# Kernel tuning notes

Hardware: AMD Instinct MI355X
Metric: run time of the kernel (lower is better)

The kernel has to match this reference:

```python
import jax, jax.numpy as jnp
import numpy as np

VOCAB, EMB, WIN = 32000, 300, 5
H1, H2, NY, NZ = 300, 300, 128, 128
B, S = 32, 512


def setup_inputs() -> dict:
    key = jax.random.key(0)
    ks = jax.random.split(key, 16)
    sc = 0.05
    inp = {
        "x": jax.random.randint(ks[0], (B, S, WIN), 0, VOCAB),
        "emb": jax.random.normal(ks[1], (VOCAB, EMB), jnp.float32) * sc,
        "W_ih1": jax.random.normal(ks[2], (H1, EMB * WIN), jnp.float32) * sc,
        "W_hh1": jax.random.normal(ks[3], (H1, H1), jnp.float32) * sc,
        "b_ih1": jax.random.normal(ks[4], (H1,), jnp.float32) * sc,
        "b_hh1": jax.random.normal(ks[5], (H1,), jnp.float32) * sc,
        "W_ih2": jax.random.normal(ks[6], (H2, H1), jnp.float32) * sc,
        "W_hh2": jax.random.normal(ks[7], (H2, H2), jnp.float32) * sc,
        "b_ih2": jax.random.normal(ks[8], (H2,), jnp.float32) * sc,
        "b_hh2": jax.random.normal(ks[9], (H2,), jnp.float32) * sc,
        "fc1_w": jax.random.normal(ks[10], (NY, H1), jnp.float32) * sc,
        "fc1_b": jax.random.normal(ks[11], (NY,), jnp.float32) * sc,
        "fc2_w": jax.random.normal(ks[12], (NZ, H2), jnp.float32) * sc,
        "fc2_b": jax.random.normal(ks[13], (NZ,), jnp.float32) * sc,
    }
    return inp


def reference(x, emb, W_ih1, W_hh1, b_ih1, b_hh1, W_ih2, W_hh2, b_ih2, b_hh2,
              fc1_w, fc1_b, fc2_w, fc2_b):
    b, s, w = x.shape
    xe = emb[jnp.transpose(x, (1, 0, 2))].reshape(s, b, w * emb.shape[1])
    xe = jax.nn.relu(xe)

    h1_0 = jnp.zeros((b, W_hh1.shape[0]), xe.dtype)
    h2_0 = jnp.zeros((b, W_hh2.shape[0]), xe.dtype)

    def step(carry, xt):
        h1, h2 = carry
        h1 = jnp.tanh(xt @ W_ih1.T + b_ih1 + h1 @ W_hh1.T + b_hh1)
        h2 = jnp.tanh(h1 @ W_ih2.T + b_ih2 + h2 @ W_hh2.T + b_hh2)
        return (h1, h2), (h1, h2)

    _, (out1, out2) = jax.lax.scan(step, (h1_0, h2_0), xe)  # [S,B,H]

    out1 = jnp.transpose(out1, (1, 0, 2)).reshape(b * s, -1)
    out2 = jnp.transpose(out2, (1, 0, 2)).reshape(b * s, -1)
    out1 = out1 @ fc1_w.T + fc1_b
    out2 = out2 @ fc2_w.T + fc2_b
    return (out1, out2)
```

## Files before the change

### kernel.cpp

```cpp
#include <hip/hip_runtime.h>
#include <hip/hip_fp16.h>

#define S_LEN 512
#define BATCH 32
#define CHUNK 16

typedef _Float16 hv2  __attribute__((ext_vector_type(2)));
typedef _Float16 half8 __attribute__((ext_vector_type(8)));
typedef float    f32x4 __attribute__((ext_vector_type(4)));

__device__ __forceinline__ float dot2f(hv2 a, hv2 b, float c) {
#if __has_builtin(__builtin_amdgcn_fdot2)
    return __builtin_amdgcn_fdot2(a, b, c, false);
#else
    return c + (float)a.x * (float)b.x + (float)a.y * (float)b.y;
#endif
}

__device__ __forceinline__ float fast_tanh(float x) {
    float e = __expf(2.f * x);
    return 1.f - 2.f / (e + 1.f);
}

__device__ __forceinline__ void lds_barrier() {
    __asm__ volatile("s_waitcnt lgkmcnt(0)\n\ts_barrier" ::: "memory");
}
__device__ __forceinline__ void vm_drain() {
    __asm__ volatile("s_waitcnt vmcnt(0)" ::: "memory");
}

#define F_GC0 64

#define E8   1280000
#define W18  64000
#define W28  12800
#define FF8  5120
#define PREP_TOTAL8 (E8 + W18 + W28 + FF8 + FF8)

__global__ __launch_bounds__(256) void k_prep(
    const float* __restrict__ emb,  const float* __restrict__ Wih1,
    const float* __restrict__ Wih2, const float* __restrict__ fc1w,
    const float* __restrict__ fc2w,
    _Float16* __restrict__ embf, _Float16* __restrict__ Wf1,
    _Float16* __restrict__ Wf2,  _Float16* __restrict__ F1,
    _Float16* __restrict__ F2,   unsigned int* __restrict__ flags)
{
    int gid = blockIdx.x * 256 + threadIdx.x;
    if (gid < 128) flags[gid] = 0u;
    if (gid >= PREP_TOTAL8) return;

    half8 v;
    _Float16* dst;

    if (gid < E8) {
        int row = gid / 40, c8 = (gid - row * 40) * 8;
        #pragma unroll
        for (int j = 0; j < 8; ++j) {
            int c = c8 + j;
            float f = (c < 300) ? emb[(size_t)row * 300 + c] : 0.f;
            v[j] = (_Float16)(f > 0.f ? f : 0.f);
        }
        dst = embf + (size_t)gid * 8;
    } else if (gid < E8 + W18) {
        int i = gid - E8;
        int row = i / 200, c8 = (i - row * 200) * 8;
        #pragma unroll
        for (int j = 0; j < 8; ++j) {
            int c = c8 + j, w = c / 320, cc = c - w * 320;
            float f = (row < 300 && cc < 300) ? Wih1[(size_t)row * 1500 + w * 300 + cc] : 0.f;
            v[j] = (_Float16)f;
        }
        dst = Wf1 + (size_t)i * 8;
    } else if (gid < E8 + W18 + W28) {
        int i = gid - E8 - W18;
        int row = i / 40, c8 = (i - row * 40) * 8;
        #pragma unroll
        for (int j = 0; j < 8; ++j) {
            int c = c8 + j;
            float f = (row < 300 && c < 300) ? Wih2[(size_t)row * 300 + c] : 0.f;
            v[j] = (_Float16)f;
        }
        dst = Wf2 + (size_t)i * 8;
    } else if (gid < E8 + W18 + W28 + FF8) {
        int i = gid - E8 - W18 - W28;
        int row = i / 40, c8 = (i - row * 40) * 8;
        #pragma unroll
        for (int j = 0; j < 8; ++j) {
            int c = c8 + j;
            v[j] = (_Float16)((c < 300) ? fc1w[(size_t)row * 300 + c] : 0.f);
        }
        dst = F1 + (size_t)i * 8;
    } else {
        int i = gid - E8 - W18 - W28 - FF8;
        int row = i / 40, c8 = (i - row * 40) * 8;
        #pragma unroll
        for (int j = 0; j < 8; ++j) {
            int c = c8 + j;
            v[j] = (_Float16)((c < 300) ? fc2w[(size_t)row * 300 + c] : 0.f);
        }
        dst = F2 + (size_t)i * 8;
    }
    *(half8*)dst = v;
}

#define LDS_BYTES 52096
#define NREC 64
#define NGEMM 76

__device__ __forceinline__ void load_u_regs(float* up, const float* __restrict__ U1,
                                            int b, int t0) {
    #pragma unroll
    for (int j = 0; j < 10; ++j) {
        int e = threadIdx.x + 512 * j;
        int row = e / 300, col = e - row * 300;
        up[j] = (e < 4800) ? U1[((size_t)((t0 + row) * BATCH + b)) * 300 + col] : 0.f;
    }
}

__device__ __forceinline__ void wait_gemm(unsigned int* flags, int c) {
    if (threadIdx.x == 0) {
        while (__hip_atomic_load(&flags[F_GC0 + c], __ATOMIC_ACQUIRE,
                                 __HIP_MEMORY_SCOPE_AGENT) < (unsigned)NGEMM)
            __builtin_amdgcn_s_sleep(2);
    }
    __syncthreads();
}

__device__ __forceinline__ void fc_epilogue(
    const _Float16 (*hc)[320], const _Float16* __restrict__ F,
    const float* __restrict__ fb, float* __restrict__ out,
    int b, int tb, int wid, int lm, int lq)
{
    f32x4 acc = (f32x4){0.f, 0.f, 0.f, 0.f};
    const int n = wid * 16 + lm;
    const _Float16* frow = F + (size_t)n * 320;
    #pragma unroll
    for (int k0 = 0; k0 < 320; k0 += 32) {
        half8 a  = *(const half8*)&hc[lm][k0 + lq * 8];
        half8 bf = *(const half8*)&frow[k0 + lq * 8];
        acc = __builtin_amdgcn_mfma_f32_16x16x32_f16(a, bf, acc, 0, 0, 0);
    }
    const float bv = fb[n];
    #pragma unroll
    for (int reg = 0; reg < 4; ++reg) {
        const int t = tb + lq * 4 + reg;
        out[(size_t)(b * 512 + t) * 128 + n] = acc[reg] + bv;
    }
}

__global__ __launch_bounds__(512) void k_rec_fused(
    const int* __restrict__ x, const _Float16* __restrict__ embf,
    const _Float16* __restrict__ Wf1,
    const float* __restrict__ bih1, const float* __restrict__ bhh1,
    float* __restrict__ U1, const float* __restrict__ Whh1,
    const _Float16* __restrict__ Wf2, const float* __restrict__ Whh2,
    const float* __restrict__ bih2, const float* __restrict__ bhh2,
    _Float16* __restrict__ H1f,
    const _Float16* __restrict__ F1, const _Float16* __restrict__ F2,
    const float* __restrict__ fb1, const float* __restrict__ fb2,
    float* __restrict__ out1, float* __restrict__ out2,
    unsigned int* __restrict__ flags)
{
    const int tid  = threadIdx.x;

    if (blockIdx.x >= NREC) {
        const int g    = blockIdx.x - NREC;
        const int wv   = tid >> 6;
        const int lane = tid & 63;
        const int m    = lane & 15;
        const int q    = lane >> 4;
        const int nt   = g % 19;
        const int mtg  = g / 19;
        const int mt   = mtg * 8 + wv;
        const int n    = nt * 16 + m;
        const _Float16* wrowB = Wf1 + (size_t)n * 1600;
        const float bias = (n < 300) ? (bih1[n] + bhh1[n]) : 0.f;

        for (int c = 0; c < 32; ++c) {
            const int r  = c * 512 + mt * 16 + m;
            const int xb = ((r & 31) * S_LEN + (r >> 5)) * 5;
            f32x4 acc = (f32x4){0.f, 0.f, 0.f, 0.f};
            #pragma unroll
            for (int w = 0; w < 5; ++w) {
                const int idx = x[xb + w];
                const _Float16* ea = embf + (size_t)idx * 320;
                const _Float16* wb = wrowB + w * 320;
                #pragma unroll
                for (int cc = 0; cc < 10; ++cc) {
                    half8 a  = *(const half8*)(ea + cc * 32 + q * 8);
                    half8 bf = *(const half8*)(wb + cc * 32 + q * 8);
                    acc = __builtin_amdgcn_mfma_f32_16x16x32_f16(a, bf, acc, 0, 0, 0);
                }
            }
            if (n < 300) {
                #pragma unroll
                for (int reg = 0; reg < 4; ++reg) {
                    const int rr = c * 512 + mt * 16 + q * 4 + reg;
                    U1[(size_t)rr * 300 + n] = acc[reg] + bias;
                }
            }
            vm_drain();
            __syncthreads();
            if (tid == 0)
                __hip_atomic_fetch_add(&flags[F_GC0 + c], 1u,
                                       __ATOMIC_RELEASE, __HIP_MEMORY_SCOPE_AGENT);
        }
        return;
    }

    extern __shared__ char smem[];
    float   (*partials)[304] = (float(*)[304])smem;
    _Float16 (*hc)[320]      = (_Float16(*)[320])(smem + 12160);
    float   (*uc)[304]       = (float(*)[304])(smem + 22400);
    _Float16 (*h1s)[320]     = (_Float16(*)[320])(smem + 41856);

    const bool comp = tid < 500;
    const int g    = comp ? tid / 50 : 0;
    const int rt   = comp ? tid % 50 : 0;
    const int lane = tid & 63;
    const int wid  = tid >> 6;
    const int lm   = lane & 15;
    const int lq   = lane >> 4;

    for (int i = tid; i < CHUNK * 320; i += 512)
        ((_Float16*)hc)[i] = (_Float16)0.f;

    if (blockIdx.x < 32) {
        const int b = blockIdx.x;
        hv2 w1[6][16];
        if (comp) {
            #pragma unroll
            for (int i = 0; i < 6; ++i) {
                const float* wr = Whh1 + (size_t)(rt + 50 * i) * 300 + g * 32;
                #pragma unroll
                for (int j = 0; j < 16; ++j) {
                    int c0 = g * 32 + 2 * j;
                    hv2 p;
                    p.x = (c0     < 300) ? (_Float16)wr[2 * j]     : (_Float16)0.f;
                    p.y = (c0 + 1 < 300) ? (_Float16)wr[2 * j + 1] : (_Float16)0.f;
                    w1[i][j] = p;
                }
            }
        }

        wait_gemm(flags, 0);
        float upref[10];
        load_u_regs(upref, U1, b, 0);

        for (int c = 0; c < 32; ++c) {
            const int t0 = c * CHUNK;
            if (c > 0) {
                const int tb = t0 - CHUNK;
                for (int i = tid; i < CHUNK * 40; i += 512) {
                    int row = i / 40, c8 = i - row * 40;
                    half8 v = *(const half8*)&hc[row][c8 * 8];
                    *(half8*)&H1f[((size_t)((tb + row) * BATCH + b)) * 320 + c8 * 8] = v;
                }
                fc_epilogue(hc, F1, fb1, out1, b, tb, wid, lm, lq);
            }
            #pragma unroll
            for (int j = 0; j < 10; ++j) {
                int e = tid + 512 * j;
                if (e < 4800) {
                    int row = e / 300, col = e - row * 300;
                    uc[row][col] = upref[j];
                }
            }
            if (c > 0) {
                vm_drain();
                __syncthreads();
                if (tid == 0)
                    __hip_atomic_store(&flags[b], (unsigned)t0,
                                       __ATOMIC_RELEASE, __HIP_MEMORY_SCOPE_AGENT);
            }
            if (c + 1 < 32) {
                wait_gemm(flags, c + 1);
                load_u_regs(upref, U1, b, t0 + CHUNK);
            }
            lds_barrier();

            for (int s = 0; s < CHUNK; ++s) {
                if (comp) {
                    const half8* hp = (const half8*)&hc[(s - 1) & 15][g * 32];
                    float a0 = 0.f, a1 = 0.f, a2 = 0.f, a3 = 0.f, a4 = 0.f, a5 = 0.f;
                    #pragma unroll
                    for (int jj = 0; jj < 4; ++jj) {
                        half8 q8 = hp[jj];
                        const hv2* qv = (const hv2*)&q8;
                        #pragma unroll
                        for (int j4 = 0; j4 < 4; ++j4) {
                            const int j = 4 * jj + j4;
                            a0 = dot2f(w1[0][j], qv[j4], a0);
                            a1 = dot2f(w1[1][j], qv[j4], a1);
                            a2 = dot2f(w1[2][j], qv[j4], a2);
                            a3 = dot2f(w1[3][j], qv[j4], a3);
                            a4 = dot2f(w1[4][j], qv[j4], a4);
                            a5 = dot2f(w1[5][j], qv[j4], a5);
                        }
                    }
                    partials[g][rt]       = a0;
                    partials[g][rt + 50]  = a1;
                    partials[g][rt + 100] = a2;
                    partials[g][rt + 150] = a3;
                    partials[g][rt + 200] = a4;
                    partials[g][rt + 250] = a5;
                }
                lds_barrier();
                if (tid < 300) {
                    float ssum = uc[s][tid];
                    #pragma unroll
                    for (int g2 = 0; g2 < 10; ++g2)
                        ssum += partials[g2][tid];
                    hc[s][tid] = (_Float16)fast_tanh(ssum);
                }
                lds_barrier();
            }
        }
        {
            const int tb = S_LEN - CHUNK;
            for (int i = tid; i < CHUNK * 40; i += 512) {
                int row = i / 40, c8 = i - row * 40;
                half8 v = *(const half8*)&hc[row][c8 * 8];
                *(half8*)&H1f[((size_t)((tb + row) * BATCH + b)) * 320 + c8 * 8] = v;
            }
            fc_epilogue(hc, F1, fb1, out1, b, tb, wid, lm, lq);
            vm_drain();
            __syncthreads();
            if (tid == 0)
                __hip_atomic_store(&flags[b], (unsigned)S_LEN,
                                   __ATOMIC_RELEASE, __HIP_MEMORY_SCOPE_AGENT);
        }
    } else {
        const int b = blockIdx.x - 32;
        hv2 whh[6][16];
        if (comp) {
            #pragma unroll
            for (int i = 0; i < 6; ++i) {
                const float* wr = Whh2 + (size_t)(rt + 50 * i) * 300 + g * 32;
                #pragma unroll
                for (int j = 0; j < 16; ++j) {
                    int c0 = g * 32 + 2 * j;
                    hv2 p;
                    p.x = (c0     < 300) ? (_Float16)wr[2 * j]     : (_Float16)0.f;
                    p.y = (c0 + 1 < 300) ? (_Float16)wr[2 * j + 1] : (_Float16)0.f;
                    whh[i][j] = p;
                }
            }
        }
        float bias = (tid < 300) ? (bih2[tid] + bhh2[tid]) : 0.f;

        for (int c = 0; c < 32; ++c) {
            const int t0 = c * CHUNK;
            if (c > 0) {
                fc_epilogue(hc, F2, fb2, out2, b, t0 - CHUNK, wid, lm, lq);
            }
            if (tid == 0) {
                while (__hip_atomic_load(&flags[b], __ATOMIC_ACQUIRE,
                                         __HIP_MEMORY_SCOPE_AGENT) < (unsigned)(t0 + CHUNK))
                    __builtin_amdgcn_s_sleep(2);
            }
            __syncthreads();

            for (int i = tid; i < CHUNK * 40; i += 512) {
                int row = i / 40, c8 = i - row * 40;
                *(half8*)&h1s[row][c8 * 8] =
                    *(const half8*)&H1f[((size_t)((t0 + row) * BATCH + b)) * 320 + c8 * 8];
            }
            lds_barrier();

            for (int nt = wid; nt < 19; nt += 8) {
                f32x4 acc = (f32x4){0.f, 0.f, 0.f, 0.f};
                const int n = nt * 16 + lm;
                const _Float16* wrow = Wf2 + (size_t)n * 320;
                #pragma unroll
                for (int k0 = 0; k0 < 320; k0 += 32) {
                    half8 a  = *(const half8*)&h1s[lm][k0 + lq * 8];
                    half8 bf = *(const half8*)&wrow[k0 + lq * 8];
                    acc = __builtin_amdgcn_mfma_f32_16x16x32_f16(a, bf, acc, 0, 0, 0);
                }
                #pragma unroll
                for (int reg = 0; reg < 4; ++reg)
                    uc[lq * 4 + reg][n] = acc[reg];
            }
            lds_barrier();

            for (int s = 0; s < CHUNK; ++s) {
                if (comp) {
                    const half8* hp = (const half8*)&hc[(s - 1) & 15][g * 32];
                    float a0 = 0.f, a1 = 0.f, a2 = 0.f, a3 = 0.f, a4 = 0.f, a5 = 0.f;
                    #pragma unroll
                    for (int jj = 0; jj < 4; ++jj) {
                        half8 q8 = hp[jj];
                        const hv2* qv = (const hv2*)&q8;
                        #pragma unroll
                        for (int j4 = 0; j4 < 4; ++j4) {
                            const int j = 4 * jj + j4;
                            a0 = dot2f(whh[0][j], qv[j4], a0);
                            a1 = dot2f(whh[1][j], qv[j4], a1);
                            a2 = dot2f(whh[2][j], qv[j4], a2);
                            a3 = dot2f(whh[3][j], qv[j4], a3);
                            a4 = dot2f(whh[4][j], qv[j4], a4);
                            a5 = dot2f(whh[5][j], qv[j4], a5);
                        }
                    }
                    partials[g][rt]       = a0;
                    partials[g][rt + 50]  = a1;
                    partials[g][rt + 100] = a2;
                    partials[g][rt + 150] = a3;
                    partials[g][rt + 200] = a4;
                    partials[g][rt + 250] = a5;
                }
                lds_barrier();
                if (tid < 300) {
                    float ssum = bias + uc[s][tid];
                    #pragma unroll
                    for (int g2 = 0; g2 < 10; ++g2)
                        ssum += partials[g2][tid];
                    hc[s][tid] = (_Float16)fast_tanh(ssum);
                }
                lds_barrier();
            }
        }
        fc_epilogue(hc, F2, fb2, out2, b, S_LEN - CHUNK, wid, lm, lq);
    }
}

extern "C" void kernel_launch(void* const* d_in, const int* in_sizes, int n_in,
                              void* d_out, int out_size, void* d_ws, size_t ws_size,
                              hipStream_t stream) {
    const int*   x     = (const int*)d_in[0];
    const float* emb   = (const float*)d_in[1];
    const float* Wih1  = (const float*)d_in[2];
    const float* Whh1  = (const float*)d_in[3];
    const float* bih1  = (const float*)d_in[4];
    const float* bhh1  = (const float*)d_in[5];
    const float* Wih2  = (const float*)d_in[6];
    const float* Whh2  = (const float*)d_in[7];
    const float* bih2  = (const float*)d_in[8];
    const float* bhh2  = (const float*)d_in[9];
    const float* fc1w  = (const float*)d_in[10];
    const float* fc1b  = (const float*)d_in[11];
    const float* fc2w  = (const float*)d_in[12];
    const float* fc2b  = (const float*)d_in[13];

    float* out1 = (float*)d_out;
    float* out2 = out1 + (size_t)16384 * 128;

    char* w = (char*)d_ws;
    unsigned int* flags = (unsigned int*)w;
    float*        U1    = (float*)(w + 512);
    _Float16*     H1    = (_Float16*)(w + 19661312);
    _Float16*     Wf1   = (_Float16*)(w + 30147072);
    _Float16*     Wf2   = (_Float16*)(w + 31171072);
    _Float16*     F1    = (_Float16*)(w + 31375872);
    _Float16*     F2    = (_Float16*)(w + 31457792);
    _Float16*     EMBF  = (_Float16*)(w + 31539712);

    const int prep_blocks = (PREP_TOTAL8 + 255) / 256;
    k_prep<<<prep_blocks, 256, 0, stream>>>(emb, Wih1, Wih2, fc1w, fc2w,
                                            EMBF, Wf1, Wf2, F1, F2, flags);

    k_rec_fused<<<NREC + NGEMM, 512, LDS_BYTES, stream>>>(
        x, EMBF, Wf1, bih1, bhh1, U1, Whh1, Wf2, Whh2, bih2, bhh2, H1,
        F1, F2, fc1b, fc2b, out1, out2, flags);
}
```

Baseline: 804.8 us.

## Stage gathered embedding rows in LDS and reassign producer GEMM blocks per M-tile

```diff
diff --git a/kernel.cpp b/kernel.cpp
--- a/kernel.cpp
+++ b/kernel.cpp
@@ -105,7 +105,7 @@
 
 #define LDS_BYTES 52096
 #define NREC 64
-#define NGEMM 76
+#define NGEMM 32
 
 __device__ __forceinline__ void load_u_regs(float* up, const float* __restrict__ U1,
                                             int b, int t0) {
@@ -162,41 +162,50 @@
     unsigned int* __restrict__ flags)
 {
     const int tid  = threadIdx.x;
+    extern __shared__ char smem[];
 
     if (blockIdx.x >= NREC) {
-        const int g    = blockIdx.x - NREC;
+        const int mt   = blockIdx.x - NREC;
         const int wv   = tid >> 6;
         const int lane = tid & 63;
         const int m    = lane & 15;
         const int q    = lane >> 4;
-        const int nt   = g % 19;
-        const int mtg  = g / 19;
-        const int mt   = mtg * 8 + wv;
-        const int n    = nt * 16 + m;
-        const _Float16* wrowB = Wf1 + (size_t)n * 1600;
-        const float bias = (n < 300) ? (bih1[n] + bhh1[n]) : 0.f;
+        _Float16 (*Asm)[1608] = (_Float16(*)[1608])smem;
 
         for (int c = 0; c < 32; ++c) {
-            const int r  = c * 512 + mt * 16 + m;
-            const int xb = ((r & 31) * S_LEN + (r >> 5)) * 5;
-            f32x4 acc = (f32x4){0.f, 0.f, 0.f, 0.f};
             #pragma unroll
-            for (int w = 0; w < 5; ++w) {
-                const int idx = x[xb + w];
-                const _Float16* ea = embf + (size_t)idx * 320;
-                const _Float16* wb = wrowB + w * 320;
+            for (int e0 = 0; e0 < 7; ++e0) {
+                const int e = tid + e0 * 512;
+                if (e < 3200) {
+                    const int i  = e / 200;
+                    const int re = e - i * 200;
+                    const int w  = re / 40;
+                    const int k8 = re - w * 40;
+                    const int r  = c * 512 + mt * 16 + i;
+                    const int idx = x[((r & 31) * S_LEN + (r >> 5)) * 5 + w];
+                    half8 v = *(const half8*)(embf + (size_t)idx * 320 + k8 * 8);
+                    *(half8*)&Asm[i][w * 320 + k8 * 8] = v;
+                }
+            }
+            lds_barrier();
+
+            for (int nt = wv; nt < 19; nt += 8) {
+                const int n = nt * 16 + m;
+                const _Float16* wrowB = Wf1 + (size_t)n * 1600;
+                f32x4 acc = (f32x4){0.f, 0.f, 0.f, 0.f};
                 #pragma unroll
-                for (int cc = 0; cc < 10; ++cc) {
-                    half8 a  = *(const half8*)(ea + cc * 32 + q * 8);
-                    half8 bf = *(const half8*)(wb + cc * 32 + q * 8);
+                for (int kt = 0; kt < 50; ++kt) {
+                    half8 a  = *(const half8*)&Asm[m][kt * 32 + q * 8];
+                    half8 bf = *(const half8*)&wrowB[kt * 32 + q * 8];
                     acc = __builtin_amdgcn_mfma_f32_16x16x32_f16(a, bf, acc, 0, 0, 0);
                 }
-            }
-            if (n < 300) {
-                #pragma unroll
-                for (int reg = 0; reg < 4; ++reg) {
-                    const int rr = c * 512 + mt * 16 + q * 4 + reg;
-                    U1[(size_t)rr * 300 + n] = acc[reg] + bias;
+                if (n < 300) {
+                    const float bias = bih1[n] + bhh1[n];
+                    #pragma unroll
+                    for (int reg = 0; reg < 4; ++reg) {
+                        const int rr = c * 512 + mt * 16 + q * 4 + reg;
+                        U1[(size_t)rr * 300 + n] = acc[reg] + bias;
+                    }
                 }
             }
             vm_drain();
@@ -208,7 +217,6 @@
         return;
     }
 
-    extern __shared__ char smem[];
     float   (*partials)[304] = (float(*)[304])smem;
     _Float16 (*hc)[320]      = (_Float16(*)[320])(smem + 12160);
     float   (*uc)[304]       = (float(*)[304])(smem + 22400);
```

Measured after the change: 1.541 ms. 91.5% more time.

## Fuse weight/embedding prep into persistent recurrent kernel with flag barrier

Applied to the files above, without the earlier changes.

```diff
diff --git a/kernel.cpp b/kernel.cpp
--- a/kernel.cpp
+++ b/kernel.cpp
@@ -30,6 +30,7 @@
 }
 
 #define F_GC0 64
+#define F_PREP 127
 
 #define E8   1280000
 #define W18  64000
@@ -37,75 +38,74 @@
 #define FF8  5120
 #define PREP_TOTAL8 (E8 + W18 + W28 + FF8 + FF8)
 
-__global__ __launch_bounds__(256) void k_prep(
+#define LDS_BYTES 52096
+#define NREC 64
+#define NGEMM 76
+#define NBLK (NREC + NGEMM)
+
+__device__ void prep_slice(
     const float* __restrict__ emb,  const float* __restrict__ Wih1,
     const float* __restrict__ Wih2, const float* __restrict__ fc1w,
     const float* __restrict__ fc2w,
     _Float16* __restrict__ embf, _Float16* __restrict__ Wf1,
     _Float16* __restrict__ Wf2,  _Float16* __restrict__ F1,
-    _Float16* __restrict__ F2,   unsigned int* __restrict__ flags)
+    _Float16* __restrict__ F2)
 {
-    int gid = blockIdx.x * 256 + threadIdx.x;
-    if (gid < 128) flags[gid] = 0u;
-    if (gid >= PREP_TOTAL8) return;
-
-    half8 v;
-    _Float16* dst;
-
-    if (gid < E8) {
-        int row = gid / 40, c8 = (gid - row * 40) * 8;
-        #pragma unroll
-        for (int j = 0; j < 8; ++j) {
-            int c = c8 + j;
-            float f = (c < 300) ? emb[(size_t)row * 300 + c] : 0.f;
-            v[j] = (_Float16)(f > 0.f ? f : 0.f);
-        }
-        dst = embf + (size_t)gid * 8;
-    } else if (gid < E8 + W18) {
-        int i = gid - E8;
-        int row = i / 200, c8 = (i - row * 200) * 8;
-        #pragma unroll
-        for (int j = 0; j < 8; ++j) {
-            int c = c8 + j, w = c / 320, cc = c - w * 320;
-            float f = (row < 300 && cc < 300) ? Wih1[(size_t)row * 1500 + w * 300 + cc] : 0.f;
-            v[j] = (_Float16)f;
-        }
-        dst = Wf1 + (size_t)i * 8;
-    } else if (gid < E8 + W18 + W28) {
-        int i = gid - E8 - W18;
-        int row = i / 40, c8 = (i - row * 40) * 8;
-        #pragma unroll
-        for (int j = 0; j < 8; ++j) {
-            int c = c8 + j;
-            float f = (row < 300 && c < 300) ? Wih2[(size_t)row * 300 + c] : 0.f;
-            v[j] = (_Float16)f;
-        }
-        dst = Wf2 + (size_t)i * 8;
-    } else if (gid < E8 + W18 + W28 + FF8) {
-        int i = gid - E8 - W18 - W28;
-        int row = i / 40, c8 = (i - row * 40) * 8;
-        #pragma unroll
-        for (int j = 0; j < 8; ++j) {
-            int c = c8 + j;
-            v[j] = (_Float16)((c < 300) ? fc1w[(size_t)row * 300 + c] : 0.f);
-        }
-        dst = F1 + (size_t)i * 8;
-    } else {
-        int i = gid - E8 - W18 - W28 - FF8;
-        int row = i / 40, c8 = (i - row * 40) * 8;
-        #pragma unroll
-        for (int j = 0; j < 8; ++j) {
-            int c = c8 + j;
-            v[j] = (_Float16)((c < 300) ? fc2w[(size_t)row * 300 + c] : 0.f);
-        }
-        dst = F2 + (size_t)i * 8;
-    }
-    *(half8*)dst = v;
-}
-
-#define LDS_BYTES 52096
-#define NREC 64
-#define NGEMM 76
+    for (int gid = blockIdx.x * 512 + threadIdx.x; gid < PREP_TOTAL8;
+         gid += NBLK * 512) {
+        half8 v;
+        _Float16* dst;
+        if (gid < E8) {
+            int row = gid / 40, c8 = (gid - row * 40) * 8;
+            #pragma unroll
+            for (int j = 0; j < 8; ++j) {
+                int c = c8 + j;
+                float f = (c < 300) ? emb[(size_t)row * 300 + c] : 0.f;
+                v[j] = (_Float16)(f > 0.f ? f : 0.f);
+            }
+            dst = embf + (size_t)gid * 8;
+        } else if (gid < E8 + W18) {
+            int i = gid - E8;
+            int row = i / 200, c8 = (i - row * 200) * 8;
+            #pragma unroll
+            for (int j = 0; j < 8; ++j) {
+                int c = c8 + j, w = c / 320, cc = c - w * 320;
+                float f = (row < 300 && cc < 300) ? Wih1[(size_t)row * 1500 + w * 300 + cc] : 0.f;
+                v[j] = (_Float16)f;
+            }
+            dst = Wf1 + (size_t)i * 8;
+        } else if (gid < E8 + W18 + W28) {
+            int i = gid - E8 - W18;
+            int row = i / 40, c8 = (i - row * 40) * 8;
+            #pragma unroll
+            for (int j = 0; j < 8; ++j) {
+                int c = c8 + j;
+                float f = (row < 300 && c < 300) ? Wih2[(size_t)row * 300 + c] : 0.f;
+                v[j] = (_Float16)f;
+            }
+            dst = Wf2 + (size_t)i * 8;
+        } else if (gid < E8 + W18 + W28 + FF8) {
+            int i = gid - E8 - W18 - W28;
+            int row = i / 40, c8 = (i - row * 40) * 8;
+            #pragma unroll
+            for (int j = 0; j < 8; ++j) {
+                int c = c8 + j;
+                v[j] = (_Float16)((c < 300) ? fc1w[(size_t)row * 300 + c] : 0.f);
+            }
+            dst = F1 + (size_t)i * 8;
+        } else {
+            int i = gid - E8 - W18 - W28 - FF8;
+            int row = i / 40, c8 = (i - row * 40) * 8;
+            #pragma unroll
+            for (int j = 0; j < 8; ++j) {
+                int c = c8 + j;
+                v[j] = (_Float16)((c < 300) ? fc2w[(size_t)row * 300 + c] : 0.f);
+            }
+            dst = F2 + (size_t)i * 8;
+        }
+        *(half8*)dst = v;
+    }
+}
 
 __device__ __forceinline__ void load_u_regs(float* up, const float* __restrict__ U1,
                                             int b, int t0) {
@@ -149,21 +149,44 @@
 }
 
 __global__ __launch_bounds__(512) void k_rec_fused(
-    const int* __restrict__ x, const _Float16* __restrict__ embf,
-    const _Float16* __restrict__ Wf1,
+    const int* __restrict__ x,
+    const float* __restrict__ emb, const float* __restrict__ Wih1f32,
+    const float* __restrict__ Wih2f32,
+    const float* __restrict__ fc1w, const float* __restrict__ fc2w,
+    _Float16* __restrict__ embf, _Float16* __restrict__ Wf1w,
+    _Float16* __restrict__ Wf2w, _Float16* __restrict__ F1w,
+    _Float16* __restrict__ F2w,
     const float* __restrict__ bih1, const float* __restrict__ bhh1,
     float* __restrict__ U1, const float* __restrict__ Whh1,
-    const _Float16* __restrict__ Wf2, const float* __restrict__ Whh2,
+    const float* __restrict__ Whh2,
     const float* __restrict__ bih2, const float* __restrict__ bhh2,
     _Float16* __restrict__ H1f,
-    const _Float16* __restrict__ F1, const _Float16* __restrict__ F2,
     const float* __restrict__ fb1, const float* __restrict__ fb2,
     float* __restrict__ out1, float* __restrict__ out2,
     unsigned int* __restrict__ flags)
 {
     const int tid  = threadIdx.x;
 
+    prep_slice(emb, Wih1f32, Wih2f32, fc1w, fc2w, embf, Wf1w, Wf2w, F1w, F2w);
+    vm_drain();
+    __syncthreads();
+    if (tid == 0)
+        __hip_atomic_fetch_add(&flags[F_PREP], 1u,
+                               __ATOMIC_RELEASE, __HIP_MEMORY_SCOPE_AGENT);
+
+    const _Float16* Wf1 = Wf1w;
+    const _Float16* Wf2 = Wf2w;
+    const _Float16* F1  = F1w;
+    const _Float16* F2  = F2w;
+
     if (blockIdx.x >= NREC) {
+        if (tid == 0) {
+            while (__hip_atomic_load(&flags[F_PREP], __ATOMIC_ACQUIRE,
+                                     __HIP_MEMORY_SCOPE_AGENT) < (unsigned)NBLK)
+                __builtin_amdgcn_s_sleep(2);
+        }
+        __syncthreads();
+
         const int g    = blockIdx.x - NREC;
         const int wv   = tid >> 6;
         const int lane = tid & 63;
@@ -456,11 +479,10 @@
     _Float16*     F2    = (_Float16*)(w + 31457792);
     _Float16*     EMBF  = (_Float16*)(w + 31539712);
 
-    const int prep_blocks = (PREP_TOTAL8 + 255) / 256;
-    k_prep<<<prep_blocks, 256, 0, stream>>>(emb, Wih1, Wih2, fc1w, fc2w,
-                                            EMBF, Wf1, Wf2, F1, F2, flags);
-
-    k_rec_fused<<<NREC + NGEMM, 512, LDS_BYTES, stream>>>(
-        x, EMBF, Wf1, bih1, bhh1, U1, Whh1, Wf2, Whh2, bih2, bhh2, H1,
-        F1, F2, fc1b, fc2b, out1, out2, flags);
-}
+    hipMemsetAsync(flags, 0, 512, stream);
+
+    k_rec_fused<<<NBLK, 512, LDS_BYTES, stream>>>(
+        x, emb, Wih1, Wih2, fc1w, fc2w, EMBF, Wf1, Wf2, F1, F2,
+        bih1, bhh1, U1, Whh1, Whh2, bih2, bhh2, H1,
+        fc1b, fc2b, out1, out2, flags);
+}
```

Measured after the change: 999.4 us. 24.2% more time.
